# Kernel optimization log

Hardware: AMD Instinct MI355X
Metric: run time of the kernel (lower is better)

The kernel has to match this reference:

```python
import jax, jax.numpy as jnp
import numpy as np
import math

HIDDEN = 1024
HEADS = 16
HEAD = HIDDEN // HEADS  # 64
SCALE_BASE = 512.0


def _gammas(heads):
    # 1 - exp(linspace(log(1/32), log(1/512), heads))
    return 1.0 - jnp.exp(jnp.linspace(math.log(1.0 / 32.0), math.log(1.0 / 512.0), heads))


def _xpos(x, downscale):
    # x: [B, H, S, d]  (same head_size d for every head -> shared tables)
    S, d = x.shape[2], x.shape[3]
    half = d // 2
    base_scale = (jnp.arange(0, d, 2, dtype=jnp.float32) + 0.4 * d) / (1.4 * d)  # [half]
    pos = jnp.arange(S, dtype=jnp.float32)
    scale = base_scale[None, :] ** (pos / SCALE_BASE)[:, None]  # [S, half]
    if downscale:
        scale = 1.0 / scale
    inv_freq = 1.0 / (10000.0 ** (jnp.arange(half, dtype=jnp.float32) / half))
    sinusoid = pos[:, None] * inv_freq[None, :]  # [S, half]
    # duplicate-interleave (each column repeated twice)
    sin = jnp.repeat(jnp.sin(sinusoid) * scale, 2, axis=-1)  # [S, d]
    cos = jnp.repeat(jnp.cos(sinusoid) * scale, 2, axis=-1)  # [S, d]
    x1 = x[..., ::2]
    x2 = x[..., 1::2]
    rot = jnp.stack([-x2, x1], axis=-1).reshape(x.shape)  # rotate_every_two
    return x * cos + rot * sin


def _decay_mask(S, gammas):
    # D[h, n, m] = gamma_h^(n-m) for n >= m else 0
    n = jnp.arange(S)[:, None]
    m = jnp.arange(S)[None, :]
    diff = (n - m).astype(jnp.float32)
    mask = (n >= m)
    pw = jnp.maximum(diff, 0.0)[None, :, :]  # avoid overflow on negative diffs
    return jnp.where(mask[None, :, :], gammas[:, None, None] ** pw, 0.0)  # [H, S, S]


def retention_forward(Q, K, V):
    B, S, _ = Q.shape
    # split heads: [B, S, HIDDEN] -> [B, H, S, HEAD]
    def split(x, hd):
        return x.reshape(B, S, HEADS, hd).transpose(0, 2, 1, 3)
    q = _xpos(split(Q, HEAD), downscale=False)
    k = _xpos(split(K, HEAD), downscale=True)
    v = split(V, HEAD)
    D = _decay_mask(S, _gammas(HEADS).astype(Q.dtype))  # [H, S, S]
    scores = jnp.einsum('bhsd,bhtd->bhst', q, k) * D[None]
    out = jnp.einsum('bhst,bhtd->bhsd', scores, v)
    return out.transpose(0, 2, 1, 3).reshape(B, S, HEADS * HEAD)


def setup_inputs() -> dict:
    key = jax.random.key(0)
    kq, kk, kv = jax.random.split(key, 3)
    B, S = 2, 2048
    return {
        'Q': jax.random.normal(kq, (B, S, HIDDEN), dtype=jnp.float32),
        'K': jax.random.normal(kk, (B, S, HIDDEN), dtype=jnp.float32),
        'V': jax.random.normal(kv, (B, S, HIDDEN), dtype=jnp.float32),
    }


def reference(Q, K, V):
    return retention_forward(Q, K, V)
```

## Files before the change

### kernel.cpp

```cpp
#include <hip/hip_runtime.h>
#include <hip/hip_bf16.h>
#include <math.h>

#define B_  2
#define S_  2048
#define H_  16
#define D_  64
#define SST 40

typedef __attribute__((ext_vector_type(8))) short bf16x8_t;
typedef __attribute__((ext_vector_type(4))) float f32x4_t;

__device__ __forceinline__ unsigned short f2bf(float f) {
    __hip_bfloat16 h = __float2bfloat16(f);
    return __builtin_bit_cast(unsigned short, h);
}

__device__ __forceinline__ void async16(const unsigned short* g, unsigned short* l) {
    __builtin_amdgcn_global_load_lds(
        (const __attribute__((address_space(1))) unsigned int*)g,
        (__attribute__((address_space(3))) unsigned int*)l, 16, 0, 0);
}

#define WAITV2 asm volatile("s_waitcnt vmcnt(2)" ::: "memory")
#define WAITV0 asm volatile("s_waitcnt vmcnt(0)" ::: "memory")
#define BAR    asm volatile("s_barrier" ::: "memory")

__global__ __launch_bounds__(256) void prep_kernel(const float* __restrict__ Q,
                                                   const float* __restrict__ K,
                                                   const float* __restrict__ V,
                                                   unsigned short* __restrict__ qb,
                                                   unsigned short* __restrict__ kb,
                                                   unsigned short* __restrict__ vt) {
    __shared__ float tile[64 * 65];
    int t   = threadIdx.x;
    int bh  = blockIdx.x >> 4;
    int scn = blockIdx.x & 15;
    int b = bh >> 4, hh = bh & 15;
    int s0 = scn * 128;

    float lnv   = -3.4657359027997265f + (float)hh * (-0.18483924814931874f);
    float gamma = 1.0f - expf(lnv);
    float l2g   = log2f(gamma);

#pragma unroll
    for (int it = 0; it < 16; ++it) {
        int idx = it * 256 + t;
        int i  = idx & 31;
        int sl = idx >> 5;
        int s  = s0 + sl;
        float pos = (float)s;

        float bsc  = (2.0f * (float)i + 25.6f) / 89.6f;
        float xsc  = exp2f(log2f(bsc) * pos * (1.0f / 512.0f));
        float invf = exp2f(-(float)i * (13.287712379549449f / 32.0f));
        float ang  = pos * invf;
        float kq = rintf(ang * 0.15915494309189535f);
        float r  = fmaf(kq, -6.2831853071795865f, ang);
        float sn = sinf(r), cs = cosf(r);

        float gs  = exp2f(pos * l2g);
        float gsi = exp2f(-pos * l2g);
        float rxs = 1.0f / xsc;

        float cq = cs * xsc * gs,  sq = sn * xsc * gs;
        float ck = cs * rxs * gsi, sk = sn * rxs * gsi;

        long inIdx = ((long)(b * S_ + s)) * 1024 + hh * 64 + 2 * i;
        float2 xq = *(const float2*)(Q + inIdx);
        float2 xk = *(const float2*)(K + inIdx);
        float q0 = xq.x * cq - xq.y * sq, q1 = xq.y * cq + xq.x * sq;
        float k0 = xk.x * ck - xk.y * sk, k1 = xk.y * ck + xk.x * sk;

        long outIdx = ((long)(bh * S_ + s)) * 64 + 2 * i;
        *(unsigned int*)(qb + outIdx) = (unsigned)f2bf(q0) | ((unsigned)f2bf(q1) << 16);
        *(unsigned int*)(kb + outIdx) = (unsigned)f2bf(k0) | ((unsigned)f2bf(k1) << 16);
    }

#pragma unroll
    for (int half = 0; half < 2; ++half) {
        __syncthreads();
        int sb = s0 + half * 64;
#pragma unroll
        for (int it = 0; it < 4; ++it) {
            int f  = it * 256 + t;
            int sl = f >> 4;
            int d4 = f & 15;
            float4 v = *(const float4*)(V + ((long)(b * S_ + sb + sl)) * 1024 + hh * 64 + d4 * 4);
            tile[sl * 65 + d4 * 4 + 0] = v.x;
            tile[sl * 65 + d4 * 4 + 1] = v.y;
            tile[sl * 65 + d4 * 4 + 2] = v.z;
            tile[sl * 65 + d4 * 4 + 3] = v.w;
        }
        __syncthreads();
        int d = t >> 2, c = t & 3;
        unsigned int pk[8];
#pragma unroll
        for (int jj = 0; jj < 8; ++jj) {
            float f0 = tile[(c * 16 + 2 * jj + 0) * 65 + d];
            float f1 = tile[(c * 16 + 2 * jj + 1) * 65 + d];
            pk[jj] = (unsigned int)f2bf(f0) | ((unsigned int)f2bf(f1) << 16);
        }
        unsigned short* outp = vt + ((long)(bh * 64 + d)) * S_ + sb + c * 16;
        ((uint4*)outp)[0] = make_uint4(pk[0], pk[1], pk[2], pk[3]);
        ((uint4*)outp)[1] = make_uint4(pk[4], pk[5], pk[6], pk[7]);
    }
}

__global__ __launch_bounds__(512, 4) void retention_kernel(const unsigned short* __restrict__ qb,
                                                           const unsigned short* __restrict__ kb,
                                                           const unsigned short* __restrict__ vt,
                                                           float* __restrict__ out) {
    __shared__ __align__(16) unsigned short KV[16384];
    __shared__ __align__(16) unsigned short Ss[8][32 * SST];
    unsigned short* K0 = KV;
    unsigned short* V0 = KV + 4096;
    unsigned short* K1 = KV + 8192;
    unsigned short* V1 = KV + 12288;

    int t = threadIdx.x;
    int w = t >> 6, lane = t & 63, quad = lane >> 4, l16 = lane & 15;
    int qw = w & 3;
    int p  = w >> 2;

    int i  = blockIdx.x;
    int g  = 15 - (i >> 5);
    int bh = i & 31;
    int b = bh >> 4, hh = bh & 15;

    int q0w  = g * 128 + qw * 32;
    int dkt  = 2 * g + (qw >> 1);
    int odd  = qw & 1;
    int kvend = 2 * g + 2;

    const unsigned short* qB = qb + ((long)bh * S_ + q0w) * 64;
    const unsigned short* kB = kb + (long)bh * S_ * 64;
    const unsigned short* vB = vt + (long)bh * 64 * S_;

    bf16x8_t aQ[2][2];
#pragma unroll
    for (int m = 0; m < 2; ++m)
#pragma unroll
        for (int kk = 0; kk < 2; ++kk)
            aQ[m][kk] = *(const bf16x8_t*)(qB + (m * 16 + l16) * 64 + kk * 32 + quad * 8);

    f32x4_t acc[2][4];
#pragma unroll
    for (int m = 0; m < 2; ++m)
#pragma unroll
        for (int nd = 0; nd < 4; ++nd) acc[m][nd] = (f32x4_t){0.f, 0.f, 0.f, 0.f};

    auto stage = [&](unsigned short* Kd, unsigned short* Vd, int kt) {
        const unsigned short* kSrc = kB + kt * 4096;
        const unsigned short* vSrc = vB + kt * 64;
        int row = w * 8 + (lane >> 3);
        int c   = (lane & 7) ^ (row & 7);
        async16(kSrc + row * 64 + c * 8, Kd + w * 512);
        async16(vSrc + (long)row * S_ + c * 8, Vd + w * 512);
    };

    auto computeHalf = [&](const unsigned short* Kt, const unsigned short* Vt, bool diag) {
        f32x4_t sc[2][2];
#pragma unroll
        for (int m = 0; m < 2; ++m)
#pragma unroll
            for (int ntl = 0; ntl < 2; ++ntl) sc[m][ntl] = (f32x4_t){0.f, 0.f, 0.f, 0.f};

#pragma unroll
        for (int kk = 0; kk < 2; ++kk)
#pragma unroll
            for (int ntl = 0; ntl < 2; ++ntl) {
                int krow = p * 32 + ntl * 16 + l16;
                bf16x8_t bk = *(const bf16x8_t*)&Kt[krow * 64 +
                                                   (((kk * 4 + quad) ^ (krow & 7)) * 8)];
                sc[0][ntl] = __builtin_amdgcn_mfma_f32_16x16x32_bf16(aQ[0][kk], bk, sc[0][ntl], 0, 0, 0);
                sc[1][ntl] = __builtin_amdgcn_mfma_f32_16x16x32_bf16(aQ[1][kk], bk, sc[1][ntl], 0, 0, 0);
            }

        unsigned short* ssw = Ss[w];
        if (!diag) {
#pragma unroll
            for (int m = 0; m < 2; ++m)
#pragma unroll
                for (int ntl = 0; ntl < 2; ++ntl)
#pragma unroll
                    for (int r = 0; r < 4; ++r)
                        ssw[(m * 16 + quad * 4 + r) * SST + ntl * 16 + l16] = f2bf(sc[m][ntl][r]);
        } else {
#pragma unroll
            for (int m = 0; m < 2; ++m)
#pragma unroll
                for (int ntl = 0; ntl < 2; ++ntl) {
                    int dlt = (m - ntl) * 16;
#pragma unroll
                    for (int r = 0; r < 4; ++r) {
                        int rr = quad * 4 + r;
                        float v = ((rr + dlt) >= l16) ? sc[m][ntl][r] : 0.0f;
                        ssw[(m * 16 + rr) * SST + ntl * 16 + l16] = f2bf(v);
                    }
                }
        }

        bf16x8_t aS0 = *(const bf16x8_t*)&ssw[(0 * 16 + l16) * SST + quad * 8];
        bf16x8_t aS1 = *(const bf16x8_t*)&ssw[(1 * 16 + l16) * SST + quad * 8];
#pragma unroll
        for (int nd = 0; nd < 4; ++nd) {
            int vrow = nd * 16 + l16;
            bf16x8_t bv = *(const bf16x8_t*)&Vt[vrow * 64 +
                                               (((p * 4 + quad) ^ (vrow & 7)) * 8)];
            acc[0][nd] = __builtin_amdgcn_mfma_f32_16x16x32_bf16(aS0, bv, acc[0][nd], 0, 0, 0);
            acc[1][nd] = __builtin_amdgcn_mfma_f32_16x16x32_bf16(aS1, bv, acc[1][nd], 0, 0, 0);
        }
    };

    stage(K0, V0, 0);
    for (int kt = 0; kt < kvend; kt += 2) {
        stage(K1, V1, kt + 1);
        WAITV2;
        BAR;
        if (kt < dkt || (kt == dkt && p <= odd)) computeHalf(K0, V0, kt == dkt && p == odd);
        BAR;

        if (kt + 2 < kvend) { stage(K0, V0, kt + 2); WAITV2; }
        else                { WAITV0; }
        BAR;
        if (kt + 1 < dkt || (kt + 1 == dkt && p <= odd))
            computeHalf(K1, V1, kt + 1 == dkt && p == odd);
        BAR;
    }

    float* red = (float*)KV;
    if (p == 1) {
#pragma unroll
        for (int m = 0; m < 2; ++m)
#pragma unroll
            for (int nd = 0; nd < 4; ++nd)
#pragma unroll
                for (int r = 0; r < 4; ++r)
                    red[qw * 2048 + (m * 16 + quad * 4 + r) * 64 + nd * 16 + l16] = acc[m][nd][r];
    }
    BAR;
    if (p == 0) {
#pragma unroll
        for (int m = 0; m < 2; ++m)
#pragma unroll
            for (int nd = 0; nd < 4; ++nd)
#pragma unroll
                for (int r = 0; r < 4; ++r) {
                    int row = q0w + m * 16 + quad * 4 + r;
                    float v = acc[m][nd][r] +
                              red[qw * 2048 + (m * 16 + quad * 4 + r) * 64 + nd * 16 + l16];
                    out[((long)(b * S_ + row)) * 1024 + hh * 64 + nd * 16 + l16] = v;
                }
    }
}

extern "C" void kernel_launch(void* const* d_in, const int* in_sizes, int n_in,
                              void* d_out, int out_size, void* d_ws, size_t ws_size,
                              hipStream_t stream) {
    const float* Q = (const float*)d_in[0];
    const float* K = (const float*)d_in[1];
    const float* V = (const float*)d_in[2];
    float* out = (float*)d_out;

    const size_t perBuf = (size_t)B_ * H_ * S_ * D_;
    unsigned short* qb = (unsigned short*)d_ws;
    unsigned short* kb = qb + perBuf;
    unsigned short* vt = kb + perBuf;

    hipLaunchKernelGGL(prep_kernel, dim3(512), dim3(256), 0, stream, Q, K, V, qb, kb, vt);
    hipLaunchKernelGGL(retention_kernel, dim3(512), dim3(512), 0, stream, qb, kb, vt, out);
}
```

Baseline: 134.4 us.

## Precompute xpos/decay tables and split prep into finer Q/K and V blocks

Adds a table kernel that computes the rotary sin/cos times xpos scale per position and frequency, plus the per-head gamma powers, once. The prep kernel then reads these tables instead of evaluating transcendentals per element. Prep is also split into 2048 Q/K blocks and 1024 V-transpose blocks with float4 loads, replacing the previous 512 blocks. This adds one kernel launch and extra table memory traffic, and falls back to using the output buffer for the tables when the workspace is too small.

After: 128.7 us. 1.04x faster.

```diff
diff --git a/kernel.cpp b/kernel.cpp
--- a/kernel.cpp
+++ b/kernel.cpp
@@ -26,67 +26,91 @@
 #define WAITV0 asm volatile("s_waitcnt vmcnt(0)" ::: "memory")
 #define BAR    asm volatile("s_barrier" ::: "memory")
 
+__global__ __launch_bounds__(256) void table_kernel(float4* __restrict__ rot4,
+                                                    float2* __restrict__ g2) {
+    int tid = blockIdx.x * 256 + threadIdx.x;
+    int i   = tid & 31;
+    int s   = tid >> 5;
+    float pos = (float)s;
+
+    float bsc  = (2.0f * (float)i + 25.6f) / 89.6f;
+    float xsc  = exp2f(log2f(bsc) * pos * (1.0f / 512.0f));
+    float invf = exp2f(-(float)i * (13.287712379549449f / 32.0f));
+    float ang  = pos * invf;
+    float kq = rintf(ang * 0.15915494309189535f);
+    float r  = fmaf(kq, -6.2831853071795865f, ang);
+    float sn = sinf(r), cs = cosf(r);
+    float rxs = 1.0f / xsc;
+    rot4[tid] = make_float4(cs * xsc, sn * xsc, cs * rxs, sn * rxs);
+
+    if (tid < H_ * S_) {
+        int hh = tid >> 11, ss = tid & 2047;
+        float lnv   = -3.4657359027997265f + (float)hh * (-0.18483924814931874f);
+        float l2g   = log2f(1.0f - expf(lnv));
+        g2[tid] = make_float2(exp2f((float)ss * l2g), exp2f(-(float)ss * l2g));
+    }
+}
+
 __global__ __launch_bounds__(256) void prep_kernel(const float* __restrict__ Q,
                                                    const float* __restrict__ K,
                                                    const float* __restrict__ V,
+                                                   const float4* __restrict__ rot4,
+                                                   const float2* __restrict__ g2,
                                                    unsigned short* __restrict__ qb,
                                                    unsigned short* __restrict__ kb,
                                                    unsigned short* __restrict__ vt) {
     __shared__ float tile[64 * 65];
     int t   = threadIdx.x;
-    int bh  = blockIdx.x >> 4;
-    int scn = blockIdx.x & 15;
-    int b = bh >> 4, hh = bh & 15;
-    int s0 = scn * 128;
-
-    float lnv   = -3.4657359027997265f + (float)hh * (-0.18483924814931874f);
-    float gamma = 1.0f - expf(lnv);
-    float l2g   = log2f(gamma);
-
-#pragma unroll
-    for (int it = 0; it < 16; ++it) {
-        int idx = it * 256 + t;
-        int i  = idx & 31;
-        int sl = idx >> 5;
-        int s  = s0 + sl;
-        float pos = (float)s;
-
-        float bsc  = (2.0f * (float)i + 25.6f) / 89.6f;
-        float xsc  = exp2f(log2f(bsc) * pos * (1.0f / 512.0f));
-        float invf = exp2f(-(float)i * (13.287712379549449f / 32.0f));
-        float ang  = pos * invf;
-        float kq = rintf(ang * 0.15915494309189535f);
-        float r  = fmaf(kq, -6.2831853071795865f, ang);
-        float sn = sinf(r), cs = cosf(r);
-
-        float gs  = exp2f(pos * l2g);
-        float gsi = exp2f(-pos * l2g);
-        float rxs = 1.0f / xsc;
-
-        float cq = cs * xsc * gs,  sq = sn * xsc * gs;
-        float ck = cs * rxs * gsi, sk = sn * rxs * gsi;
-
-        long inIdx = ((long)(b * S_ + s)) * 1024 + hh * 64 + 2 * i;
-        float2 xq = *(const float2*)(Q + inIdx);
-        float2 xk = *(const float2*)(K + inIdx);
-        float q0 = xq.x * cq - xq.y * sq, q1 = xq.y * cq + xq.x * sq;
-        float k0 = xk.x * ck - xk.y * sk, k1 = xk.y * ck + xk.x * sk;
-
-        long outIdx = ((long)(bh * S_ + s)) * 64 + 2 * i;
-        *(unsigned int*)(qb + outIdx) = (unsigned)f2bf(q0) | ((unsigned)f2bf(q1) << 16);
-        *(unsigned int*)(kb + outIdx) = (unsigned)f2bf(k0) | ((unsigned)f2bf(k1) << 16);
-    }
-
-#pragma unroll
-    for (int half = 0; half < 2; ++half) {
-        __syncthreads();
-        int sb = s0 + half * 64;
+    int bid = blockIdx.x;
+
+    if (bid < 2048) {
+        int bh = bid & 31;
+        int b = bh >> 4, hh = bh & 15;
+        int s0 = (bid >> 5) * 32;
+
+#pragma unroll
+        for (int it = 0; it < 2; ++it) {
+            int idx = it * 256 + t;
+            int i8  = idx & 15;
+            int sl  = idx >> 4;
+            int s   = s0 + sl;
+
+            float4 r0 = rot4[s * 32 + 2 * i8];
+            float4 r1 = rot4[s * 32 + 2 * i8 + 1];
+            float2 g  = g2[hh * 2048 + s];
+
+            long inIdx = ((long)(b * S_ + s)) * 1024 + hh * 64 + 4 * i8;
+            float4 xq = *(const float4*)(Q + inIdx);
+            float4 xk = *(const float4*)(K + inIdx);
+
+            float cq0 = r0.x * g.x, sq0 = r0.y * g.x;
+            float ck0 = r0.z * g.y, sk0 = r0.w * g.y;
+            float cq1 = r1.x * g.x, sq1 = r1.y * g.x;
+            float ck1 = r1.z * g.y, sk1 = r1.w * g.y;
+
+            float q0 = xq.x * cq0 - xq.y * sq0, q1 = xq.y * cq0 + xq.x * sq0;
+            float q2 = xq.z * cq1 - xq.w * sq1, q3 = xq.w * cq1 + xq.z * sq1;
+            float k0 = xk.x * ck0 - xk.y * sk0, k1 = xk.y * ck0 + xk.x * sk0;
+            float k2 = xk.z * ck1 - xk.w * sk1, k3 = xk.w * ck1 + xk.z * sk1;
+
+            long outIdx = ((long)(bh * S_ + s)) * 64 + 4 * i8;
+            *(uint2*)(qb + outIdx) = make_uint2((unsigned)f2bf(q0) | ((unsigned)f2bf(q1) << 16),
+                                                (unsigned)f2bf(q2) | ((unsigned)f2bf(q3) << 16));
+            *(uint2*)(kb + outIdx) = make_uint2((unsigned)f2bf(k0) | ((unsigned)f2bf(k1) << 16),
+                                                (unsigned)f2bf(k2) | ((unsigned)f2bf(k3) << 16));
+        }
+    } else {
+        int vb = bid - 2048;
+        int bh = vb & 31;
+        int b = bh >> 4, hh = bh & 15;
+        int s0 = (vb >> 5) * 64;
+
 #pragma unroll
         for (int it = 0; it < 4; ++it) {
             int f  = it * 256 + t;
             int sl = f >> 4;
             int d4 = f & 15;
-            float4 v = *(const float4*)(V + ((long)(b * S_ + sb + sl)) * 1024 + hh * 64 + d4 * 4);
+            float4 v = *(const float4*)(V + ((long)(b * S_ + s0 + sl)) * 1024 + hh * 64 + d4 * 4);
             tile[sl * 65 + d4 * 4 + 0] = v.x;
             tile[sl * 65 + d4 * 4 + 1] = v.y;
             tile[sl * 65 + d4 * 4 + 2] = v.z;
@@ -101,7 +125,7 @@
             float f1 = tile[(c * 16 + 2 * jj + 1) * 65 + d];
             pk[jj] = (unsigned int)f2bf(f0) | ((unsigned int)f2bf(f1) << 16);
         }
-        unsigned short* outp = vt + ((long)(bh * 64 + d)) * S_ + sb + c * 16;
+        unsigned short* outp = vt + ((long)(bh * 64 + d)) * S_ + s0 + c * 16;
         ((uint4*)outp)[0] = make_uint4(pk[0], pk[1], pk[2], pk[3]);
         ((uint4*)outp)[1] = make_uint4(pk[4], pk[5], pk[6], pk[7]);
     }
@@ -268,6 +292,15 @@
     unsigned short* kb = qb + perBuf;
     unsigned short* vt = kb + perBuf;
 
-    hipLaunchKernelGGL(prep_kernel, dim3(512), dim3(256), 0, stream, Q, K, V, qb, kb, vt);
+    const size_t bufBytes = 3 * perBuf * sizeof(unsigned short);
+    const size_t tblBytes = (size_t)S_ * 32 * sizeof(float4) + (size_t)H_ * S_ * sizeof(float2);
+    char* tbl;
+    if (ws_size >= bufBytes + tblBytes) tbl = (char*)d_ws + bufBytes;
+    else                                tbl = (char*)d_out;
+    float4* rot4 = (float4*)tbl;
+    float2* g2   = (float2*)(rot4 + (size_t)S_ * 32);
+
+    hipLaunchKernelGGL(table_kernel, dim3(256), dim3(256), 0, stream, rot4, g2);
+    hipLaunchKernelGGL(prep_kernel, dim3(3072), dim3(256), 0, stream, Q, K, V, rot4, g2, qb, kb, vt);
     hipLaunchKernelGGL(retention_kernel, dim3(512), dim3(512), 0, stream, qb, kb, vt, out);
 }
```
